# Performance work log

Hardware: AMD Instinct MI355X
Metric: run time of the kernel (lower is better)

The kernel has to match this reference:

```python
import jax, jax.numpy as jnp
import numpy as np
from jax import lax

B, N, D, E, P, K, H = 32, 512, 512, 8, 96, 25, 4
PAD = 12  # conv padding so length is preserved


def setup_inputs() -> dict:
    key = jax.random.key(0)
    ks = jax.random.split(key, 16)
    s = 0.05  # weight scale to keep softmax/cosine well-conditioned
    x = jax.random.normal(ks[0], (B, N, D), dtype=jnp.float32)
    router = jax.random.normal(ks[1], (1, E, D), dtype=jnp.float32)
    Wq = jax.random.normal(ks[2], (D, D), dtype=jnp.float32) * s
    bq = jax.random.normal(ks[3], (D,), dtype=jnp.float32) * s
    Wk = jax.random.normal(ks[4], (D, D), dtype=jnp.float32) * s
    bk = jax.random.normal(ks[5], (D,), dtype=jnp.float32) * s
    Wv = jax.random.normal(ks[6], (D, D), dtype=jnp.float32) * s
    bv = jax.random.normal(ks[7], (D,), dtype=jnp.float32) * s
    Wo = jax.random.normal(ks[8], (D, D), dtype=jnp.float32) * s
    bo = jax.random.normal(ks[9], (D,), dtype=jnp.float32) * s
    Wc = jax.random.normal(ks[10], (E, 2, K), dtype=jnp.float32) * s  # E experts' Conv1d(2,1,25) stacked as out-channels
    bc = jax.random.normal(ks[11], (E,), dtype=jnp.float32) * s
    Wp = jax.random.normal(ks[12], (E, D, P), dtype=jnp.float32) * s  # E experts' Linear(D,P), stored (in,out)
    bp = jax.random.normal(ks[13], (E, P), dtype=jnp.float32) * s
    return {"x": x, "router": router, "Wq": Wq, "bq": bq, "Wk": Wk, "bk": bk,
            "Wv": Wv, "bv": bv, "Wo": Wo, "bo": bo, "Wc": Wc, "bc": bc,
            "Wp": Wp, "bp": bp}


def _forward(x, router, Wq, bq, Wk, bk, Wv, bv, Wo, bo, Wc, bc, Wp, bp):
    b, n, d = x.shape
    e = router.shape[1]
    dk = d // H
    r = jnp.broadcast_to(router, (b, e, d))
    # multi-head attention: queries=router slots, keys/values=x (dropout = identity at eval)
    q = (r @ Wq + bq).reshape(b, e, H, dk)
    k = (x @ Wk + bk).reshape(b, n, H, dk)
    v = (x @ Wv + bv).reshape(b, n, H, dk)
    scale = 1.0 / jnp.sqrt(jnp.asarray(dk, x.dtype))
    scores = jnp.einsum('blhe,bshe->bhls', q, k)  # [b,H,e,n]
    A = jax.nn.softmax(scale * scores, axis=-1)
    att = jnp.einsum('bhls,bshd->blhd', A, v).reshape(b, e, d)
    att = att @ Wo + bo  # [b,e,d]
    # cosine-similarity routing score, mapped to (1+pi)/2
    dot = jnp.einsum('bed,bnd->ben', att, x)
    norm_a = jnp.linalg.norm(att, axis=2, keepdims=True)          # [b,e,1]
    norm_x = jnp.linalg.norm(x, axis=2)[:, None, :]                # [b,1,n]
    score = (1.0 + dot / (norm_a * norm_x)) / 2.0                  # [b,e,n]
    idx = jnp.argmax(score, axis=1)                                # [b,n] expert per token
    z = jnp.take_along_axis(att, idx[:, :, None], axis=1)          # [b,n,d]
    result = jnp.stack([x, z], axis=-2).reshape(b * n, 2, d)       # [bn,2,d]
    # run all E expert convs at once (experts stacked as output channels)
    conv_out = lax.conv_general_dilated(
        result, Wc, window_strides=(1,), padding=[(PAD, PAD)],
        dimension_numbers=('NCH', 'OIH', 'NCH')) + bc[None, :, None]  # [bn,E,d]
    lin = jnp.einsum('nel,elp->nep', conv_out, Wp) + bp[None]         # [bn,E,P]
    flat_idx = idx.reshape(-1)
    out = jnp.take_along_axis(lin, flat_idx[:, None, None], axis=1)[:, 0, :]
    return out.reshape(b, n, P)


def reference(x, router, Wq, bq, Wk, bk, Wv, bv, Wo, bo, Wc, bc, Wp, bp):
    return _forward(x, router, Wq, bq, Wk, bk, Wv, bv, Wo, bo, Wc, bc, Wp, bp)
```

## Files before the change

kernel.cpp:

```cpp
#include <hip/hip_runtime.h>
#include <hip/hip_bf16.h>

#define B_ 32
#define N_ 512
#define D_ 512
#define E_ 8
#define P_ 96
#define KC 25
#define H_ 4
#define DK 128
#define HE 32
#define BN 16384

typedef short short8 __attribute__((ext_vector_type(8)));
typedef float f32x4 __attribute__((ext_vector_type(4)));

#define OCNT  4096
#define OS2   4352
#define OM    5120
#define OC    21504
#define OA    21536
#define OAP   545824
#define OATT  676896
#define OTOK  807968
#define OWEFF 939040
#define OZC   1332256
#define OUP   1356832

__device__ __forceinline__ float b2f(short s) {
  unsigned u = ((unsigned)(unsigned short)s) << 16;
  return __builtin_bit_cast(float, u);
}
__device__ __forceinline__ unsigned short f2b(float f) {
  return __builtin_bit_cast(unsigned short, __float2bfloat16(f));
}

__global__ __launch_bounds__(256) void k_head(const float* __restrict__ router,
        const float* __restrict__ Wq, const float* __restrict__ bq,
        const float* __restrict__ Wk, const float* __restrict__ bk,
        const float* __restrict__ Wp, const float* __restrict__ Wc,
        float* __restrict__ M, float* __restrict__ c,
        int* __restrict__ cnt, float* __restrict__ s2,
        __hip_bfloat16* __restrict__ weff) {
  __shared__ float sm[5824];
  int bid = blockIdx.x;
  int tid = threadIdx.x;
  if (bid < 64) {
    float* rs = sm;
    float* ps = sm + 512;
    float* qs = sm + 768;
    int he = bid >> 1, ch = bid & 1;
    int h = he >> 3, e = he & 7;
    for (int i = tid; i < 512; i += 256) rs[i] = router[e * D_ + i];
    __syncthreads();
    {
      int j = tid & 127, dh = tid >> 7;
      const float* wq = Wq + h * 128 + j;
      float acc = 0.f;
      for (int d = dh * 256; d < dh * 256 + 256; d += 4) {
        acc = fmaf(rs[d], wq[d * D_], acc);
        acc = fmaf(rs[d + 1], wq[(d + 1) * D_], acc);
        acc = fmaf(rs[d + 2], wq[(d + 2) * D_], acc);
        acc = fmaf(rs[d + 3], wq[(d + 3) * D_], acc);
      }
      ps[dh * 128 + j] = acc;
    }
    __syncthreads();
    if (tid < 128) qs[tid] = ps[tid] + ps[128 + tid] + bq[h * 128 + tid];
    __syncthreads();
    {
      int d0 = ch * 256 + tid;
      const float* wrow = Wk + d0 * D_ + h * 128;
      float acc = 0.f;
      for (int jj = 0; jj < 128; jj += 4) {
        float4 wv = *(const float4*)(wrow + jj);
        acc = fmaf(wv.x, qs[jj], acc);
        acc = fmaf(wv.y, qs[jj + 1], acc);
        acc = fmaf(wv.z, qs[jj + 2], acc);
        acc = fmaf(wv.w, qs[jj + 3], acc);
      }
      M[he * D_ + d0] = acc;
    }
    if (ch == 0 && tid < 64) {
      float s = qs[tid] * bk[h * 128 + tid] + qs[tid + 64] * bk[h * 128 + tid + 64];
#pragma unroll
      for (int off = 32; off; off >>= 1) s += __shfl_xor(s, off);
      if (tid == 0) c[he] = s;
    }
  } else if (bid < 192) {
    float* T = sm;
    float* wcs = sm + 5760;
    int eb = bid - 64;
    int e = eb >> 4, mc = eb & 15;
    int lo = mc * 32 - 12;
    for (int idx = tid; idx < 56 * 24; idx += 256) {
      int lp = idx / 24, p4 = (idx - lp * 24) * 4;
      int l = lo + lp;
      float4 v = {0.f, 0.f, 0.f, 0.f};
      if (l >= 0 && l < D_) v = *(const float4*)(Wp + (e * D_ + l) * P_ + p4);
      T[p4 * 60 + lp] = v.x; T[(p4 + 1) * 60 + lp] = v.y;
      T[(p4 + 2) * 60 + lp] = v.z; T[(p4 + 3) * 60 + lp] = v.w;
    }
    if (tid < 50) wcs[tid] = Wc[e * 2 * KC + tid];
    __syncthreads();
    int m = tid & 31, pg = tid >> 5;
#pragma unroll
    for (int j = 0; j < 2; ++j)
      for (int k2 = 0; k2 < 12; ++k2) {
        int p = pg * 12 + k2;
        float acc = 0.f;
#pragma unroll
        for (int k = 0; k < KC; ++k)
          acc = fmaf(wcs[j * 25 + k], T[p * 60 + m - k + 24], acc);
        weff[(((e * 2 + j) * P_ + p) << 9) + mc * 32 + m] = __float2bfloat16(acc);
      }
  } else {
    int e = bid - 192;
    if (bid == 192) cnt[tid] = 0;
    if (tid < 192) {
      int p = tid % 96, lg = tid / 96;
      float s = 0.f;
      const float* wp = Wp + e * D_ * P_ + p;
      for (int l = lg * 256; l < lg * 256 + 256; ++l) s += wp[l * P_];
      sm[lg * 96 + p] = s;
    }
    __syncthreads();
    if (tid < 96) s2[e * 96 + tid] = sm[tid] + sm[96 + tid];
  }
}

__global__ __launch_bounds__(128) void k_logits(const float* __restrict__ x,
        const float* __restrict__ M, float* __restrict__ A0,
        float* __restrict__ A1) {
  __shared__ float xs[64 * 132];
  __shared__ float Ms[32 * 132];
  int dh = blockIdx.x & 1;
  int nt8 = (blockIdx.x >> 1) & 7;
  int b = blockIdx.x >> 4;
  int tid = threadIdx.x;
  const float* xb = x + (b * N_ + nt8 * 64) * D_ + dh * 256;
  const float* Mb = M + dh * 256;
  float acc[4][4] = {{0.f}};
  for (int kc = 0; kc < 2; ++kc) {
    for (int idx = tid; idx < 2048; idx += 128) {
      int r = idx >> 5, c4 = (idx & 31) * 4;
      *(float4*)(xs + r * 132 + c4) = *(const float4*)(xb + r * D_ + kc * 128 + c4);
    }
    for (int idx = tid; idx < 1024; idx += 128) {
      int r = idx >> 5, c4 = (idx & 31) * 4;
      *(float4*)(Ms + r * 132 + c4) = *(const float4*)(Mb + r * D_ + kc * 128 + c4);
    }
    __syncthreads();
    int nt = tid & 15, ht = tid >> 4;
#pragma unroll 4
    for (int d4 = 0; d4 < 128; d4 += 4) {
      float4 xv[4], mv[4];
#pragma unroll
      for (int i = 0; i < 4; ++i)
        xv[i] = *(const float4*)(xs + (nt + 16 * i) * 132 + d4);
#pragma unroll
      for (int j = 0; j < 4; ++j)
        mv[j] = *(const float4*)(Ms + (ht + 8 * j) * 132 + d4);
#pragma unroll
      for (int i = 0; i < 4; ++i)
#pragma unroll
        for (int j = 0; j < 4; ++j) {
          float s = acc[i][j];
          s = fmaf(xv[i].x, mv[j].x, s);
          s = fmaf(xv[i].y, mv[j].y, s);
          s = fmaf(xv[i].z, mv[j].z, s);
          s = fmaf(xv[i].w, mv[j].w, s);
          acc[i][j] = s;
        }
    }
    __syncthreads();
  }
  int nt = tid & 15, ht = tid >> 4;
  float* Ad = dh ? A1 : A0;
#pragma unroll
  for (int j = 0; j < 4; ++j) {
    int he = ht + 8 * j;
#pragma unroll
    for (int i = 0; i < 4; ++i)
      Ad[(b * HE + he) * N_ + nt8 * 64 + nt + 16 * i] = acc[i][j];
  }
}

__global__ __launch_bounds__(256) void k_softmax(float* __restrict__ A0,
        const float* __restrict__ A1, const float* __restrict__ c) {
  int row = blockIdx.x;
  float* p0 = A0 + row * N_;
  const float* p1 = A1 + row * N_;
  float cc = c[row & 31];
  int t = threadIdx.x;
  const float scale = 0.08838834764831845f;
  float v0 = scale * (p0[t] + p1[t] + cc);
  float v1 = scale * (p0[t + 256] + p1[t + 256] + cc);
  __shared__ float red[4], red2[4];
  float m = fmaxf(v0, v1);
#pragma unroll
  for (int off = 32; off; off >>= 1) m = fmaxf(m, __shfl_xor(m, off));
  if ((t & 63) == 0) red[t >> 6] = m;
  __syncthreads();
  m = fmaxf(fmaxf(red[0], red[1]), fmaxf(red[2], red[3]));
  float e0 = expf(v0 - m), e1 = expf(v1 - m);
  float s = e0 + e1;
#pragma unroll
  for (int off = 32; off; off >>= 1) s += __shfl_xor(s, off);
  if ((t & 63) == 0) red2[t >> 6] = s;
  __syncthreads();
  s = red2[0] + red2[1] + red2[2] + red2[3];
  float inv = 1.0f / s;
  p0[t] = e0 * inv;
  p0[t + 256] = e1 * inv;
}

__global__ __launch_bounds__(512) void k_u2(const float* __restrict__ x,
        const float* __restrict__ A, float* __restrict__ up) {
  __shared__ float As[64 * 33];
  int nq = blockIdx.x, b = blockIdx.y;
  for (int idx = threadIdx.x; idx < 64 * 32; idx += 512) {
    int n = idx & 63, he = idx >> 6;
    As[n * 33 + he] = A[(b * HE + he) * N_ + nq * 64 + n];
  }
  __syncthreads();
  int dq = threadIdx.x & 127, hg = threadIdx.x >> 7;
  const float* xb = x + (b * N_ + nq * 64) * D_ + dq * 4;
  float acc[8][4];
#pragma unroll
  for (int j = 0; j < 8; ++j)
#pragma unroll
    for (int k = 0; k < 4; ++k) acc[j][k] = 0.f;
  for (int n = 0; n < 64; ++n) {
    float4 xv = *(const float4*)(xb + n * D_);
    const float* ar = As + n * 33 + hg * 8;
#pragma unroll
    for (int j = 0; j < 8; ++j) {
      float a = ar[j];
      acc[j][0] = fmaf(a, xv.x, acc[j][0]);
      acc[j][1] = fmaf(a, xv.y, acc[j][1]);
      acc[j][2] = fmaf(a, xv.z, acc[j][2]);
      acc[j][3] = fmaf(a, xv.w, acc[j][3]);
    }
  }
  float* o = up + (((b * 8 + nq) * HE) + hg * 8) * D_ + dq * 4;
#pragma unroll
  for (int j = 0; j < 8; ++j) {
    float4 v; v.x = acc[j][0]; v.y = acc[j][1]; v.z = acc[j][2]; v.w = acc[j][3];
    *(float4*)(o + j * D_) = v;
  }
}

__global__ __launch_bounds__(256) void k_attpre(const float* __restrict__ up,
        const float* __restrict__ Wv, const float* __restrict__ bv,
        float* __restrict__ ap) {
  __shared__ float us[8 * D_];
  int e = blockIdx.x & 7;
  int ic = (blockIdx.x >> 3) & 3;
  int bq = blockIdx.x >> 5;
  for (int idx = threadIdx.x; idx < 8 * 128; idx += 256) {
    int rr = idx >> 7, d4 = (idx & 127) * 4;
    const float* base = up + (((bq * 8 + rr) * 8) * HE + ic * 8 + e) * D_ + d4;
    float4 s = {0.f, 0.f, 0.f, 0.f};
#pragma unroll
    for (int nq = 0; nq < 8; ++nq) {
      float4 v = *(const float4*)(base + nq * HE * D_);
      s.x += v.x; s.y += v.y; s.z += v.z; s.w += v.w;
    }
    *(float4*)(us + rr * D_ + d4) = s;
  }
  __syncthreads();
  int i = ic * 128 + (threadIdx.x & 127);
  int bg = threadIdx.x >> 7;
  const float* usb = us + bg * 4 * D_;
  float acc[4] = {0.f, 0.f, 0.f, 0.f};
  for (int d = 0; d < D_; d += 4) {
    float w0 = Wv[(d + 0) * D_ + i];
    float w1 = Wv[(d + 1) * D_ + i];
    float w2 = Wv[(d + 2) * D_ + i];
    float w3 = Wv[(d + 3) * D_ + i];
#pragma unroll
    for (int r = 0; r < 4; ++r) {
      float4 uv = *(const float4*)(usb + r * D_ + d);
      float s = acc[r];
      s = fmaf(uv.x, w0, s); s = fmaf(uv.y, w1, s);
      s = fmaf(uv.z, w2, s); s = fmaf(uv.w, w3, s);
      acc[r] = s;
    }
  }
  float bvi = bv[i];
#pragma unroll
  for (int r = 0; r < 4; ++r)
    ap[((bq * 8 + bg * 4 + r) * E_ + e) * D_ + i] = acc[r] + bvi;
}

__global__ __launch_bounds__(256) void k_att(const float* __restrict__ ap,
        const float* __restrict__ Wo, const float* __restrict__ bo,
        float* __restrict__ att) {
  __shared__ float ps[8 * D_];
  int b = blockIdx.x >> 2, oc = blockIdx.x & 3;
  for (int idx = threadIdx.x; idx < 8 * D_; idx += 256)
    ps[idx] = ap[b * E_ * D_ + idx];
  __syncthreads();
  int o = oc * 128 + (threadIdx.x & 127);
  int eg = threadIdx.x >> 7;
  const float* pe = ps + eg * 4 * D_;
  float acc[4] = {0.f, 0.f, 0.f, 0.f};
  for (int i2 = 0; i2 < D_; i2 += 4) {
    float w0 = Wo[(i2 + 0) * D_ + o];
    float w1 = Wo[(i2 + 1) * D_ + o];
    float w2 = Wo[(i2 + 2) * D_ + o];
    float w3 = Wo[(i2 + 3) * D_ + o];
#pragma unroll
    for (int r = 0; r < 4; ++r) {
      float4 pv = *(const float4*)(pe + r * D_ + i2);
      float s = acc[r];
      s = fmaf(pv.x, w0, s); s = fmaf(pv.y, w1, s);
      s = fmaf(pv.z, w2, s); s = fmaf(pv.w, w3, s);
      acc[r] = s;
    }
  }
  float boo = bo[o];
#pragma unroll
  for (int r = 0; r < 4; ++r)
    att[(b * E_ + eg * 4 + r) * D_ + o] = acc[r] + boo;
}

__global__ __launch_bounds__(256) void k_route2(const float* __restrict__ x,
        const float* __restrict__ att, const __hip_bfloat16* __restrict__ weff,
        const float* __restrict__ s2, const float* __restrict__ bc,
        const float* __restrict__ bp, int* __restrict__ cnt,
        int* __restrict__ tok, float* __restrict__ zc) {
  __shared__ float att_s[8 * D_];
  __shared__ float rn[8];
  __shared__ float red[4][520];
  __shared__ int blist[8][32];
  __shared__ int bcnt[8];
  int b = blockIdx.x >> 4, tile = blockIdx.x & 15;
  for (int idx = threadIdx.x; idx < 1024; idx += 256)
    *(float4*)(att_s + idx * 4) = *(const float4*)(att + b * E_ * D_ + idx * 4);
  if (threadIdx.x < 8) bcnt[threadIdx.x] = 0;
  __syncthreads();
  {
    int e = threadIdx.x >> 5, l = threadIdx.x & 31;
    float s = 0.f;
    for (int d0 = l; d0 < D_; d0 += 32) {
      float v = att_s[e * D_ + d0];
      s = fmaf(v, v, s);
    }
#pragma unroll
    for (int off = 16; off; off >>= 1) s += __shfl_xor(s, off);
    if (l == 0) rn[e] = 1.0f / sqrtf(s);
  }
  __syncthreads();
  int w = threadIdx.x >> 6, lane = threadIdx.x & 63;
  int e2 = lane & 7, ch = lane >> 3;
  float* rw = red[w];
  for (int i = 0; i < 8; ++i) {
    int t = b * N_ + tile * 32 + w * 8 + i;
    const float* xp = x + t * D_ + lane * 8;
    float4 xa = *(const float4*)xp;
    float4 xb4 = *(const float4*)(xp + 4);
    float p[8];
#pragma unroll
    for (int e = 0; e < 8; ++e) {
      const float* apt = att_s + e * D_ + lane * 8;
      float4 a0 = *(const float4*)apt;
      float4 a1 = *(const float4*)(apt + 4);
      float s = a0.x * xa.x;
      s = fmaf(a0.y, xa.y, s); s = fmaf(a0.z, xa.z, s); s = fmaf(a0.w, xa.w, s);
      s = fmaf(a1.x, xb4.x, s); s = fmaf(a1.y, xb4.y, s);
      s = fmaf(a1.z, xb4.z, s); s = fmaf(a1.w, xb4.w, s);
      p[e] = s;
    }
#pragma unroll
    for (int e = 0; e < 8; ++e) rw[e * 65 + lane] = p[e];
    float s = 0.f;
#pragma unroll
    for (int k = 0; k < 8; ++k) s += rw[e2 * 65 + ch * 8 + k];
    s += __shfl_xor(s, 8); s += __shfl_xor(s, 16); s += __shfl_xor(s, 32);
    float sc = s * rn[e2];
    int be = e2;
#pragma unroll
    for (int off = 1; off < 8; off <<= 1) {
      float o = __shfl_xor(sc, off);
      int oe = __shfl_xor(be, off);
      if (o > sc || (o == sc && oe < be)) { sc = o; be = oe; }
    }
    if (lane == 0) {
      int slot = atomicAdd(&bcnt[be], 1);
      blist[be][slot] = t;
    }
  }
  __syncthreads();
  {
    int e = threadIdx.x >> 5, r = threadIdx.x & 31;
    int ce = bcnt[e];
    int gs = 0;
    if (r == 0 && ce > 0) gs = atomicAdd(&cnt[e * 32], ce);
    gs = __shfl(gs, (threadIdx.x & 63) & 32);
    for (int k2 = r; k2 < ce; k2 += 32) tok[e * BN + gs + k2] = blist[e][k2];
  }
  int grp = threadIdx.x >> 4, l16 = threadIdx.x & 15;
  for (int r = 0; r < 3; ++r) {
    int P = tile * 48 + r * 16 + grp;
    int ez = P / 96, p = P - ez * 96;
    const short* wrow = (const short*)weff + (((ez * 2 + 1) * P_ + p) << 9);
    const float* arow = att_s + ez * D_;
    float acc = 0.f;
#pragma unroll
    for (int seg = 0; seg < 4; ++seg) {
      int d = seg * 128 + l16 * 8;
      short8 w8 = *(const short8*)(wrow + d);
      const float* a8 = arow + d;
      acc = fmaf(a8[0], b2f(w8[0]), acc); acc = fmaf(a8[1], b2f(w8[1]), acc);
      acc = fmaf(a8[2], b2f(w8[2]), acc); acc = fmaf(a8[3], b2f(w8[3]), acc);
      acc = fmaf(a8[4], b2f(w8[4]), acc); acc = fmaf(a8[5], b2f(w8[5]), acc);
      acc = fmaf(a8[6], b2f(w8[6]), acc); acc = fmaf(a8[7], b2f(w8[7]), acc);
    }
    acc += __shfl_xor(acc, 1); acc += __shfl_xor(acc, 2);
    acc += __shfl_xor(acc, 4); acc += __shfl_xor(acc, 8);
    if (l16 == 0)
      zc[(b * E_ + ez) * P_ + p] = acc + bc[ez] * s2[ez * 96 + p] + bp[ez * 96 + p];
  }
}

__global__ __launch_bounds__(256) void k_final(const float* __restrict__ x,
        const __hip_bfloat16* __restrict__ weff, const float* __restrict__ zc,
        const int* __restrict__ cnt, const int* __restrict__ tok,
        float* __restrict__ out) {
  __shared__ __align__(16) unsigned short xsb[32 * 520];
  __shared__ int toks[32];
  int g = blockIdx.x;
  int cl_e[E_], bs[E_ + 1];
  bs[0] = 0;
#pragma unroll
  for (int e = 0; e < E_; ++e) {
    cl_e[e] = cnt[e * 32];
    bs[e + 1] = bs[e] + ((cl_e[e] + 31) >> 5);
  }
  if (g >= bs[E_]) return;
  int e = 0;
#pragma unroll
  for (int k = 1; k < E_; ++k) if (g >= bs[k]) e = k;
  int base = (g - bs[e]) * 32;
  int cnt_e = cl_e[e];
  int cl = cnt_e - base; if (cl > 32) cl = 32;
  int tid = threadIdx.x;
  if (tid < 32) toks[tid] = (tid < cl) ? tok[e * BN + base + tid] : tok[e * BN + base];
  __syncthreads();
  for (int idx = tid; idx < 32 * 128; idx += 256) {
    int r = idx >> 7, c4 = (idx & 127) * 4;
    float4 v = *(const float4*)(x + toks[r] * D_ + c4);
    ushort4 u4;
    u4.x = f2b(v.x); u4.y = f2b(v.y); u4.z = f2b(v.z); u4.w = f2b(v.w);
    *(ushort4*)(xsb + r * 520 + c4) = u4;
  }
  __syncthreads();
  int wave = tid >> 6, lane = tid & 63;
  int mw = wave & 1, nw = wave >> 1;
  int m16 = lane & 15, quad = lane >> 4;
  const short* w0 = (const short*)(weff + (e * 2 + 0) * P_ * D_);
  f32x4 acc[3];
#pragma unroll
  for (int nt = 0; nt < 3; ++nt) acc[nt] = (f32x4){0.f, 0.f, 0.f, 0.f};
  const short* arow = (const short*)xsb + (mw * 16 + m16) * 520 + quad * 8;
  const short* brow = w0 + (nw * 48 + m16) * D_ + quad * 8;
  for (int kt = 0; kt < 16; ++kt) {
    int koff = kt * 32;
    short8 a = *(const short8*)(arow + koff);
#pragma unroll
    for (int nt = 0; nt < 3; ++nt) {
      short8 bf = *(const short8*)(brow + nt * 16 * D_ + koff);
      acc[nt] = __builtin_amdgcn_mfma_f32_16x16x32_bf16(a, bf, acc[nt], 0, 0, 0);
    }
  }
#pragma unroll
  for (int nt = 0; nt < 3; ++nt)
#pragma unroll
    for (int rr = 0; rr < 4; ++rr) {
      int row = mw * 16 + quad * 4 + rr;
      if (row < cl) {
        int tg = toks[row];
        int bb = tg >> 9;
        int p = nw * 48 + nt * 16 + m16;
        out[tg * P_ + p] = acc[nt][rr] + zc[(bb * E_ + e) * P_ + p];
      }
    }
}

extern "C" void kernel_launch(void* const* d_in, const int* in_sizes, int n_in,
                              void* d_out, int out_size, void* d_ws, size_t ws_size,
                              hipStream_t stream) {
  const float* x      = (const float*)d_in[0];
  const float* router = (const float*)d_in[1];
  const float* Wq     = (const float*)d_in[2];
  const float* bq     = (const float*)d_in[3];
  const float* Wk     = (const float*)d_in[4];
  const float* bk     = (const float*)d_in[5];
  const float* Wv     = (const float*)d_in[6];
  const float* bv     = (const float*)d_in[7];
  const float* Wo     = (const float*)d_in[8];
  const float* bo     = (const float*)d_in[9];
  const float* Wc     = (const float*)d_in[10];
  const float* bc     = (const float*)d_in[11];
  const float* Wp     = (const float*)d_in[12];
  const float* bp     = (const float*)d_in[13];
  float* out = (float*)d_out;
  float* w = (float*)d_ws;

  int*   cnt  = (int*)(w + OCNT);
  float* s2   = w + OS2;
  float* M    = w + OM;
  float* c    = w + OC;
  float* A0   = w + OA;
  float* A1   = w + OUP;
  float* ap   = w + OAP;
  float* att  = w + OATT;
  int*   tok  = (int*)(w + OTOK);
  __hip_bfloat16* weff = (__hip_bfloat16*)(w + OWEFF);
  float* zc   = w + OZC;
  float* up   = w + OUP;

  k_head<<<200, 256, 0, stream>>>(router, Wq, bq, Wk, bk, Wp, Wc, M, c, cnt, s2, weff);
  k_logits<<<512, 128, 0, stream>>>(x, M, A0, A1);
  k_softmax<<<1024, 256, 0, stream>>>(A0, A1, c);
  k_u2<<<dim3(8, 32), 512, 0, stream>>>(x, A0, up);
  k_attpre<<<128, 256, 0, stream>>>(up, Wv, bv, ap);
  k_att<<<128, 256, 0, stream>>>(ap, Wo, bo, att);
  k_route2<<<512, 256, 0, stream>>>(x, att, weff, s2, bc, bp, cnt, tok, zc);
  k_final<<<520, 256, 0, stream>>>(x, weff, zc, cnt, tok, out);
}
```

Baseline: 233.7 us.

## Fuse value and output projections into one kernel keeping intermediate in LDS

Merges the Wv projection kernel and the Wo projection kernel into a single kernel, one block per (expert, group of 4 batches). The intermediate per-head projected values stay in shared memory instead of going through a global workspace buffer, which saves one launch and a global round trip. The trade-off is that grid size drops from 128 to 64 blocks, leaving most CUs idle, and each thread now runs a longer serial dot-product loop.

```diff
diff --git a/kernel.cpp b/kernel.cpp
--- a/kernel.cpp
+++ b/kernel.cpp
@@ -20,7 +20,6 @@
 #define OM    5120
 #define OC    21504
 #define OA    21536
-#define OAP   545824
 #define OATT  676896
 #define OTOK  807968
 #define OWEFF 939040
@@ -251,79 +250,68 @@
   }
 }
 
-__global__ __launch_bounds__(256) void k_attpre(const float* __restrict__ up,
+__global__ __launch_bounds__(512) void k_vo(const float* __restrict__ up,
         const float* __restrict__ Wv, const float* __restrict__ bv,
-        float* __restrict__ ap) {
-  __shared__ float us[8 * D_];
-  int e = blockIdx.x & 7;
-  int ic = (blockIdx.x >> 3) & 3;
-  int bq = blockIdx.x >> 5;
-  for (int idx = threadIdx.x; idx < 8 * 128; idx += 256) {
-    int rr = idx >> 7, d4 = (idx & 127) * 4;
-    const float* base = up + (((bq * 8 + rr) * 8) * HE + ic * 8 + e) * D_ + d4;
+        const float* __restrict__ Wo, const float* __restrict__ bo,
+        float* __restrict__ att) {
+  __shared__ float us[16 * 512];
+  __shared__ float ap_s[4 * 512];
+  int e = blockIdx.x & 7, bg = blockIdx.x >> 3;
+  int tid = threadIdx.x;
+  for (int idx = tid; idx < 16 * 128; idx += 512) {
+    int r = idx >> 7, d4 = (idx & 127) * 4;
+    int h = r >> 2, bb = r & 3;
+    int b = bg * 4 + bb;
+    const float* base = up + ((b * 8) * HE + h * 8 + e) * D_ + d4;
     float4 s = {0.f, 0.f, 0.f, 0.f};
 #pragma unroll
     for (int nq = 0; nq < 8; ++nq) {
       float4 v = *(const float4*)(base + nq * HE * D_);
       s.x += v.x; s.y += v.y; s.z += v.z; s.w += v.w;
     }
-    *(float4*)(us + rr * D_ + d4) = s;
-  }
-  __syncthreads();
-  int i = ic * 128 + (threadIdx.x & 127);
-  int bg = threadIdx.x >> 7;
-  const float* usb = us + bg * 4 * D_;
-  float acc[4] = {0.f, 0.f, 0.f, 0.f};
-  for (int d = 0; d < D_; d += 4) {
-    float w0 = Wv[(d + 0) * D_ + i];
-    float w1 = Wv[(d + 1) * D_ + i];
-    float w2 = Wv[(d + 2) * D_ + i];
-    float w3 = Wv[(d + 3) * D_ + i];
-#pragma unroll
-    for (int r = 0; r < 4; ++r) {
-      float4 uv = *(const float4*)(usb + r * D_ + d);
-      float s = acc[r];
-      s = fmaf(uv.x, w0, s); s = fmaf(uv.y, w1, s);
-      s = fmaf(uv.z, w2, s); s = fmaf(uv.w, w3, s);
-      acc[r] = s;
-    }
-  }
-  float bvi = bv[i];
-#pragma unroll
-  for (int r = 0; r < 4; ++r)
-    ap[((bq * 8 + bg * 4 + r) * E_ + e) * D_ + i] = acc[r] + bvi;
-}
-
-__global__ __launch_bounds__(256) void k_att(const float* __restrict__ ap,
-        const float* __restrict__ Wo, const float* __restrict__ bo,
-        float* __restrict__ att) {
-  __shared__ float ps[8 * D_];
-  int b = blockIdx.x >> 2, oc = blockIdx.x & 3;
-  for (int idx = threadIdx.x; idx < 8 * D_; idx += 256)
-    ps[idx] = ap[b * E_ * D_ + idx];
-  __syncthreads();
-  int o = oc * 128 + (threadIdx.x & 127);
-  int eg = threadIdx.x >> 7;
-  const float* pe = ps + eg * 4 * D_;
-  float acc[4] = {0.f, 0.f, 0.f, 0.f};
-  for (int i2 = 0; i2 < D_; i2 += 4) {
-    float w0 = Wo[(i2 + 0) * D_ + o];
-    float w1 = Wo[(i2 + 1) * D_ + o];
-    float w2 = Wo[(i2 + 2) * D_ + o];
-    float w3 = Wo[(i2 + 3) * D_ + o];
-#pragma unroll
-    for (int r = 0; r < 4; ++r) {
-      float4 pv = *(const float4*)(pe + r * D_ + i2);
-      float s = acc[r];
-      s = fmaf(pv.x, w0, s); s = fmaf(pv.y, w1, s);
-      s = fmaf(pv.z, w2, s); s = fmaf(pv.w, w3, s);
-      acc[r] = s;
-    }
-  }
-  float boo = bo[o];
-#pragma unroll
-  for (int r = 0; r < 4; ++r)
-    att[(b * E_ + eg * 4 + r) * D_ + o] = acc[r] + boo;
+    *(float4*)(us + r * 512 + d4) = s;
+  }
+  __syncthreads();
+  {
+    int i = tid;
+    int h = i >> 7;
+    const float* u0 = us + (h * 4 + 0) * 512;
+    const float* u1 = us + (h * 4 + 1) * 512;
+    const float* u2 = us + (h * 4 + 2) * 512;
+    const float* u3 = us + (h * 4 + 3) * 512;
+    float a0 = 0.f, a1 = 0.f, a2 = 0.f, a3 = 0.f;
+    const float* wv = Wv + i;
+    for (int d = 0; d < 512; ++d) {
+      float w = wv[d * D_];
+      a0 = fmaf(u0[d], w, a0); a1 = fmaf(u1[d], w, a1);
+      a2 = fmaf(u2[d], w, a2); a3 = fmaf(u3[d], w, a3);
+    }
+    float bvi = bv[i];
+    ap_s[0 * 512 + i] = a0 + bvi;
+    ap_s[1 * 512 + i] = a1 + bvi;
+    ap_s[2 * 512 + i] = a2 + bvi;
+    ap_s[3 * 512 + i] = a3 + bvi;
+  }
+  __syncthreads();
+  {
+    int o = tid;
+    float a0 = 0.f, a1 = 0.f, a2 = 0.f, a3 = 0.f;
+    const float* wo = Wo + o;
+    const float* p0 = ap_s;
+    const float* p1 = ap_s + 512;
+    const float* p2 = ap_s + 1024;
+    const float* p3 = ap_s + 1536;
+    for (int i = 0; i < 512; ++i) {
+      float w = wo[i * D_];
+      a0 = fmaf(p0[i], w, a0); a1 = fmaf(p1[i], w, a1);
+      a2 = fmaf(p2[i], w, a2); a3 = fmaf(p3[i], w, a3);
+    }
+    float boo = bo[o];
+    att[((bg * 4 + 0) * E_ + e) * D_ + o] = a0 + boo;
+    att[((bg * 4 + 1) * E_ + e) * D_ + o] = a1 + boo;
+    att[((bg * 4 + 2) * E_ + e) * D_ + o] = a2 + boo;
+    att[((bg * 4 + 3) * E_ + e) * D_ + o] = a3 + boo;
+  }
 }
 
 __global__ __launch_bounds__(256) void k_route2(const float* __restrict__ x,
@@ -515,7 +503,6 @@
   float* c    = w + OC;
   float* A0   = w + OA;
   float* A1   = w + OUP;
-  float* ap   = w + OAP;
   float* att  = w + OATT;
   int*   tok  = (int*)(w + OTOK);
   __hip_bfloat16* weff = (__hip_bfloat16*)(w + OWEFF);
@@ -526,8 +513,7 @@
   k_logits<<<512, 128, 0, stream>>>(x, M, A0, A1);
   k_softmax<<<1024, 256, 0, stream>>>(A0, A1, c);
   k_u2<<<dim3(8, 32), 512, 0, stream>>>(x, A0, up);
-  k_attpre<<<128, 256, 0, stream>>>(up, Wv, bv, ap);
-  k_att<<<128, 256, 0, stream>>>(ap, Wo, bo, att);
+  k_vo<<<64, 512, 0, stream>>>(up, Wv, bv, Wo, bo, att);
   k_route2<<<512, 256, 0, stream>>>(x, att, weff, s2, bc, bp, cnt, tok, zc);
   k_final<<<520, 256, 0, stream>>>(x, weff, zc, cnt, tok, out);
 }
```

Result: slower. 246.5 us (+5.5%).
